# Performance work log

Measured on AMD Instinct MI355X. Metric: run time of the kernel, lower is better.

Reference implementation:

```python
import jax, jax.numpy as jnp
import numpy as np

SEQ, D_IN, D_OUT, RANK, N_ADAPTERS = 8192, 4096, 4096, 16, 8


def setup_inputs() -> dict:
    key = jax.random.key(0)
    ks = jax.random.split(key, 7)
    return {
        "x": jax.random.normal(ks[0], (SEQ, D_IN), jnp.float32),
        "weight": jax.random.normal(ks[1], (D_IN, D_OUT), jnp.float32) * (D_IN ** -0.5),
        "bias": jax.random.normal(ks[2], (D_OUT,), jnp.float32),
        "A_buffer": jax.random.normal(ks[3], (N_ADAPTERS, RANK, D_IN), jnp.float32) * (D_IN ** -0.5),
        "B_buffer": jax.random.normal(ks[4], (N_ADAPTERS, D_OUT, RANK), jnp.float32) * (RANK ** -0.5),
        "scalings": jax.random.uniform(ks[5], (SEQ,), jnp.float32, 0.5, 2.0),
        "token_indices": jax.random.randint(ks[6], (SEQ,), 0, N_ADAPTERS, jnp.int32),
    }


def reference(x, weight, bias, A_buffer, B_buffer, scalings, token_indices):
    # Base linear layer: [S, D_in] @ [D_in, D_out] + bias
    base_output = x @ weight + bias
    n_adapters = A_buffer.shape[0]
    delta = jnp.zeros_like(base_output)
    # Grouped LoRA GEMM: per-adapter small GEMMs, masked scatter back per token.
    for e in range(n_adapters):
        # run_lora_a_gemm: x @ A[e]^T with per-token scaling -> [S, rank]
        a_out = (x @ A_buffer[e].T) * scalings[:, None]
        # run_lora_b_gemm: a_out @ B[e]^T -> [S, D_out]
        b_out = a_out @ B_buffer[e].T
        delta = delta + jnp.where((token_indices == e)[:, None], b_out, 0.0)
    return base_output + delta
```

## Files before the change

### kernel.cpp

```cpp
#include <hip/hip_runtime.h>
#include <hip/hip_bf16.h>
#include <cstdint>

#define SEQ   8192
#define DIN   4096
#define DOUT  4096
#define RANK  16
#define NAD   8
#define KC    (DIN + NAD*RANK)

using f32x4  = __attribute__((ext_vector_type(4))) float;
using bf16x8 = __attribute__((ext_vector_type(8))) short;

__device__ __forceinline__ unsigned short f2bf(float f) {
  union { float f; uint32_t u; } v; v.f = f;
  return (unsigned short)((v.u + 0x7fffu + ((v.u >> 16) & 1u)) >> 16);
}

__device__ __forceinline__ void async_copy16(void* lds, const void* gmem) {
  __builtin_amdgcn_global_load_lds(
      (__attribute__((address_space(1))) void*)(uintptr_t)gmem,
      (__attribute__((address_space(3))) void*)(uint32_t)(uintptr_t)lds,
      16, 0, 0);
}


__global__ void cvt_x_kernel(const float* __restrict__ x, unsigned short* __restrict__ xcat) {
  const int64_t nchunks = (int64_t)SEQ * DIN / 8;
  for (int64_t c = (int64_t)blockIdx.x * blockDim.x + threadIdx.x; c < nchunks;
       c += (int64_t)gridDim.x * blockDim.x) {
    int64_t base = c * 8;
    int s = (int)(base >> 12);
    int k = (int)(base & (DIN - 1));
    float4 p = *(const float4*)(x + base);
    float4 q = *(const float4*)(x + base + 4);
    union { unsigned short h[8]; int4 v; } o;
    o.h[0]=f2bf(p.x); o.h[1]=f2bf(p.y); o.h[2]=f2bf(p.z); o.h[3]=f2bf(p.w);
    o.h[4]=f2bf(q.x); o.h[5]=f2bf(q.y); o.h[6]=f2bf(q.z); o.h[7]=f2bf(q.w);
    *(int4*)(xcat + (int64_t)s * KC + k) = o.v;
  }
}

__global__ void cvt_a_kernel(const float* __restrict__ a, unsigned short* __restrict__ abf) {
  int c = blockIdx.x * 256 + threadIdx.x;
  int64_t base = (int64_t)c * 8;
  float4 p = *(const float4*)(a + base);
  float4 q = *(const float4*)(a + base + 4);
  union { unsigned short h[8]; int4 v; } o;
  o.h[0]=f2bf(p.x); o.h[1]=f2bf(p.y); o.h[2]=f2bf(p.z); o.h[3]=f2bf(p.w);
  o.h[4]=f2bf(q.x); o.h[5]=f2bf(q.y); o.h[6]=f2bf(q.z); o.h[7]=f2bf(q.w);
  *(int4*)(abf + base) = o.v;
}

__global__ void cvt_w_kernel(const float* __restrict__ w, unsigned short* __restrict__ wcat) {
  int t  = threadIdx.x;
  int bn = blockIdx.x & 127;
  int bk = blockIdx.x >> 7;
  int n = bn * 32 + (t & 31);
  int k = bk * 64 + (t >> 5) * 8;
  union { unsigned short h[8]; int4 v; } o;
#pragma unroll
  for (int j = 0; j < 8; j++)
    o.h[j] = f2bf(w[(int64_t)(k + j) * DOUT + n]);
  *(int4*)(wcat + (int64_t)n * KC + k) = o.v;
}

__global__ void cvt_b_kernel(const float* __restrict__ Bbuf, unsigned short* __restrict__ wcat) {
  int idx = blockIdx.x * 256 + threadIdx.x;
  int n = idx >> 7, er = idx & 127;
  int e = er >> 4, r = er & 15;
  float v = Bbuf[((int64_t)e * DOUT + n) * RANK + r];
  wcat[(int64_t)n * KC + DIN + er] = f2bf(v);
}

__global__ __launch_bounds__(256) void gemm_lora_a(
    const unsigned short* __restrict__ A,
    const unsigned short* __restrict__ Bb,
    float* __restrict__ aout) {
  constexpr int BK = 64;
  __shared__ unsigned short sA[64 * BK];
  __shared__ unsigned short sB[128 * BK];
  int tid = threadIdx.x, wave = tid >> 6, lane = tid & 63;
  int quad = lane >> 4, l16 = lane & 15;
  int mb = blockIdx.x & 127;
  int sp = blockIdx.x >> 7;
  int row0 = mb * 64;
  int kbase = sp * (DIN / 2);
  int wm = wave >> 1, wn = wave & 1;
  int f8 = l16 & 7;

  const f32x4 zero = {0.f, 0.f, 0.f, 0.f};
  f32x4 acc[2][4];
#pragma unroll
  for (int i = 0; i < 2; i++)
#pragma unroll
    for (int j = 0; j < 4; j++) acc[i][j] = zero;

  for (int kt = 0; kt < (DIN / 2) / BK; ++kt) {
    int k0 = kbase + kt * BK;
#pragma unroll
    for (int i = 0; i < 2; i++) {
      int c = i * 256 + tid;
      int r = c >> 3, kc = ((c & 7) ^ (r & 7)) * 8;
      async_copy16(&sA[c * 8], A + (int64_t)(row0 + r) * KC + k0 + kc);
    }
#pragma unroll
    for (int i = 0; i < 4; i++) {
      int c = i * 256 + tid;
      int r = c >> 3, kc = ((c & 7) ^ (r & 7)) * 8;
      async_copy16(&sB[c * 8], Bb + (int64_t)r * DIN + k0 + kc);
    }
    __syncthreads();
#pragma unroll
    for (int ks = 0; ks < 2; ks++) {
      bf16x8 af[2], bfr[4];
      int qq = ks * 4 + quad;
      int qp = (qq ^ f8) * 8;
#pragma unroll
      for (int mi = 0; mi < 2; mi++)
        af[mi] = *(const bf16x8*)&sA[(wm * 32 + mi * 16 + l16) * BK + qp];
#pragma unroll
      for (int ni = 0; ni < 4; ni++)
        bfr[ni] = *(const bf16x8*)&sB[(wn * 64 + ni * 16 + l16) * BK + qp];
#pragma unroll
      for (int mi = 0; mi < 2; mi++)
#pragma unroll
        for (int ni = 0; ni < 4; ni++)
          acc[mi][ni] = __builtin_amdgcn_mfma_f32_16x16x32_bf16(af[mi], bfr[ni], acc[mi][ni], 0, 0, 0);
    }
    __syncthreads();
  }

  float* op = aout + (int64_t)sp * SEQ * 128;
#pragma unroll
  for (int ni = 0; ni < 4; ni++) {
    int er = wn * 64 + ni * 16 + l16;
#pragma unroll
    for (int mi = 0; mi < 2; mi++) {
      int s0 = row0 + wm * 32 + mi * 16 + quad * 4;
#pragma unroll
      for (int r = 0; r < 4; r++)
        op[(int64_t)(s0 + r) * 128 + er] = acc[mi][ni][r];
    }
  }
}

__global__ void lora_combine(const float* __restrict__ aout, const float* __restrict__ scal,
                             const int* __restrict__ tok, unsigned short* __restrict__ xcat) {
  int idx = blockIdx.x * 256 + threadIdx.x;
  int s = idx >> 7, er = idx & 127;
  float v = aout[idx] + aout[idx + (int64_t)SEQ * 128];
  v *= scal[s];
  v = ((er >> 4) == tok[s]) ? v : 0.0f;
  xcat[(int64_t)s * KC + DIN + er] = f2bf(v);
}


#define CFENCE asm volatile("" ::: "memory")

template<int MQ, int NQ>
__device__ __forceinline__ void ds_loads(const unsigned short* aT, const unsigned short* bT,
                                         int wm, int wn, int l16, int quad,
                                         bf16x8 (&af)[4][2], bf16x8 (&bfr)[2][2]) {
  int f8 = l16 & 7;
#pragma unroll
  for (int ks = 0; ks < 2; ks++) {
    int qp = ((ks * 4 + quad) ^ f8) * 8;
#pragma unroll
    for (int mi = 0; mi < 4; mi++)
      af[mi][ks] = *(const bf16x8*)&aT[(wm * 128 + MQ * 64 + mi * 16 + l16) * 64 + qp];
#pragma unroll
    for (int ni = 0; ni < 2; ni++)
      bfr[ni][ks] = *(const bf16x8*)&bT[(wn * 64 + NQ * 32 + ni * 16 + l16) * 64 + qp];
  }
}

template<int MQ, int NQ>
__device__ __forceinline__ void mfma_quad(f32x4 (&acc)[8][4], bf16x8 (&af)[4][2], bf16x8 (&bfr)[2][2]) {
  __builtin_amdgcn_s_setprio(1);
#pragma unroll
  for (int mi = 0; mi < 4; mi++)
#pragma unroll
    for (int ni = 0; ni < 2; ni++)
#pragma unroll
      for (int ks = 0; ks < 2; ks++)
        acc[MQ * 4 + mi][NQ * 2 + ni] = __builtin_amdgcn_mfma_f32_16x16x32_bf16(
            af[mi][ks], bfr[ni][ks], acc[MQ * 4 + mi][NQ * 2 + ni], 0, 0, 0);
  __builtin_amdgcn_s_setprio(0);
}

__device__ __forceinline__ void stage_A(unsigned short* sAb, const unsigned short* Ag,
                                        int mq, int k0, int tid) {
  int rr  = tid >> 3;
  int q8  = (tid & 7) * 8;
  int qc8 = ((tid & 7) ^ (rr & 7)) * 8;
  int r0 = mq * 64 + rr;
  async_copy16(sAb + r0 * 64 + q8, Ag + (int64_t)r0 * KC + k0 + qc8);
  int r1 = r0 + 128;
  async_copy16(sAb + r1 * 64 + q8, Ag + (int64_t)r1 * KC + k0 + qc8);
}

__device__ __forceinline__ void stage_B(unsigned short* sBb, const unsigned short* Bg,
                                        int nq, int k0, int tid) {
  int rB  = ((tid >> 3) & 31) | ((tid >> 8) << 6);
  int q8  = (tid & 7) * 8;
  int qc8 = ((tid & 7) ^ ((tid >> 3) & 7)) * 8;
  int r0 = nq * 32 + rB;
  async_copy16(sBb + r0 * 64 + q8, Bg + (int64_t)r0 * KC + k0 + qc8);
  int r1 = r0 + 128;
  async_copy16(sBb + r1 * 64 + q8, Bg + (int64_t)r1 * KC + k0 + qc8);
}

#define PHASE(MQ, NQ, aT, bT, STAGE_STMT)                        \
  ds_loads<MQ, NQ>(aT, bT, wm, wn, l16, quad, af, bfr);          \
  STAGE_STMT;                                                    \
  CFENCE; __builtin_amdgcn_s_barrier();                          \
  asm volatile("s_waitcnt lgkmcnt(0)" ::: "memory");             \
  mfma_quad<MQ, NQ>(acc, af, bfr)

#define ENDPHASE  CFENCE; __builtin_amdgcn_s_barrier(); CFENCE

__global__ __launch_bounds__(512, 2) void gemm_main8(
    const unsigned short* __restrict__ A,
    const unsigned short* __restrict__ B,
    const float* __restrict__ bias,
    float* __restrict__ out) {
  extern __shared__ unsigned short smem[];
  unsigned short* a0 = smem;
  unsigned short* b0 = smem + 16384;
  unsigned short* a1 = smem + 32768;
  unsigned short* b1 = smem + 49152;

  int tid = threadIdx.x, wave = tid >> 6, lane = tid & 63;
  int quad = lane >> 4, l16 = lane & 15;
  int wm = wave >> 2, wn = wave & 3;

  int bid = blockIdx.x;
  int cid = (bid & 7) * 64 + (bid >> 3);
  int bm = cid >> 4, bn = cid & 15;
  int row0 = bm * 256, col0 = bn * 256;

  const unsigned short* Ag = A + (int64_t)row0 * KC;
  const unsigned short* Bg = B + (int64_t)col0 * KC;

  const f32x4 zero = {0.f, 0.f, 0.f, 0.f};
  f32x4 acc[8][4];
#pragma unroll
  for (int i = 0; i < 8; i++)
#pragma unroll
    for (int j = 0; j < 4; j++) acc[i][j] = zero;

  bf16x8 af[4][2], bfr[2][2];

  stage_A(a0, Ag, 0, 0, tid);
  stage_B(b0, Bg, 0, 0, tid);
  stage_A(a0, Ag, 1, 0, tid);
  stage_B(b0, Bg, 1, 0, tid);
  stage_A(a1, Ag, 0, 64, tid);
  stage_B(b1, Bg, 0, 64, tid);
  asm volatile("s_waitcnt vmcnt(4)" ::: "memory");
  ENDPHASE;

  for (int tp = 0; tp < 32; ++tp) {
    int kE  = tp * 128;
    int kO  = kE + 64;
    int kE2 = kE + 128;
    int kO2 = kE + 192;
    PHASE(0, 0, a0, b0, stage_A(a1, Ag, 1, kO,  tid)); ENDPHASE;
    PHASE(0, 1, a0, b0, stage_B(b1, Bg, 1, kO,  tid)); ENDPHASE;
    PHASE(1, 0, a0, b0, stage_A(a0, Ag, 0, kE2, tid)); ENDPHASE;
    PHASE(1, 1, a0, b0, stage_B(b0, Bg, 0, kE2, tid));
    asm volatile("s_waitcnt vmcnt(4)" ::: "memory");
    ENDPHASE;
    PHASE(0, 0, a1, b1, stage_A(a0, Ag, 1, kE2, tid)); ENDPHASE;
    PHASE(0, 1, a1, b1, stage_B(b0, Bg, 1, kE2, tid)); ENDPHASE;
    PHASE(1, 0, a1, b1, stage_A(a1, Ag, 0, kO2, tid)); ENDPHASE;
    PHASE(1, 1, a1, b1, stage_B(b1, Bg, 0, kO2, tid));
    asm volatile("s_waitcnt vmcnt(4)" ::: "memory");
    ENDPHASE;
  }

  PHASE(0, 0, a0, b0, stage_A(a1, Ag, 1, 4160, tid)); ENDPHASE;
  PHASE(0, 1, a0, b0, stage_B(b1, Bg, 1, 4160, tid)); ENDPHASE;
  PHASE(1, 0, a0, b0, ((void)0)); ENDPHASE;
  PHASE(1, 1, a0, b0, ((void)0));
  asm volatile("s_waitcnt vmcnt(0)" ::: "memory");
  ENDPHASE;
  PHASE(0, 0, a1, b1, ((void)0)); ENDPHASE;
  PHASE(0, 1, a1, b1, ((void)0)); ENDPHASE;
  PHASE(1, 0, a1, b1, ((void)0)); ENDPHASE;
  PHASE(1, 1, a1, b1, ((void)0));

#pragma unroll
  for (int ni = 0; ni < 4; ni++) {
    int col = col0 + wn * 64 + ni * 16 + l16;
    float bv = bias[col];
#pragma unroll
    for (int mi = 0; mi < 8; mi++) {
      int rbase = row0 + wm * 128 + mi * 16 + quad * 4;
#pragma unroll
      for (int r = 0; r < 4; r++)
        out[(int64_t)(rbase + r) * DOUT + col] = acc[mi][ni][r] + bv;
    }
  }
}

__global__ void fb_aout(const float* __restrict__ x, const float* __restrict__ Abuf,
                        const float* __restrict__ scal, const int* __restrict__ tok,
                        float* __restrict__ aout) {
  int s = blockIdx.x;
  int e = tok[s];
  __shared__ float red[256];
  for (int r = 0; r < RANK; ++r) {
    float p = 0.f;
    for (int k = threadIdx.x; k < DIN; k += 256)
      p += x[(int64_t)s * DIN + k] * Abuf[((int64_t)e * RANK + r) * DIN + k];
    red[threadIdx.x] = p;
    __syncthreads();
    for (int off = 128; off > 0; off >>= 1) {
      if (threadIdx.x < off) red[threadIdx.x] += red[threadIdx.x + off];
      __syncthreads();
    }
    if (threadIdx.x == 0) aout[s * RANK + r] = red[0] * scal[s];
    __syncthreads();
  }
}
__global__ void fb_out(const float* __restrict__ x, const float* __restrict__ w,
                       const float* __restrict__ bias, const float* __restrict__ Bbuf,
                       const int* __restrict__ tok, const float* __restrict__ aout,
                       float* __restrict__ out) {
  int64_t idx = (int64_t)blockIdx.x * blockDim.x + threadIdx.x;
  int s = (int)(idx >> 12), n = (int)(idx & (DOUT - 1));
  float accv = bias[n];
  for (int k = 0; k < DIN; ++k)
    accv += x[(int64_t)s * DIN + k] * w[(int64_t)k * DOUT + n];
  int e = tok[s];
  float d = 0.f;
  for (int r = 0; r < RANK; ++r)
    d += aout[s * RANK + r] * Bbuf[((int64_t)e * DOUT + n) * RANK + r];
  out[idx] = accv + d;
}

extern "C" void kernel_launch(void* const* d_in, const int* in_sizes, int n_in,
                              void* d_out, int out_size, void* d_ws, size_t ws_size,
                              hipStream_t stream) {
  const float* x    = (const float*)d_in[0];
  const float* w    = (const float*)d_in[1];
  const float* bias = (const float*)d_in[2];
  const float* Abuf = (const float*)d_in[3];
  const float* Bbuf = (const float*)d_in[4];
  const float* scal = (const float*)d_in[5];
  const int*   tok  = (const int*)d_in[6];
  float* out = (float*)d_out;

  const size_t xcat_b = (size_t)SEQ * KC * 2;
  const size_t wcat_b = (size_t)DOUT * KC * 2;
  const size_t abf_b  = (size_t)NAD * RANK * DIN * 2;
  const size_t aout_b = (size_t)2 * SEQ * 128 * 4;

  if (ws_size >= xcat_b + wcat_b + abf_b + aout_b) {
    static bool lds_attr_done = false;
    if (!lds_attr_done) {
      (void)hipFuncSetAttribute((const void*)gemm_main8,
                                hipFuncAttributeMaxDynamicSharedMemorySize, 131072);
      lds_attr_done = true;
    }
    unsigned short* xcat = (unsigned short*)d_ws;
    unsigned short* wcat = (unsigned short*)((char*)d_ws + xcat_b);
    unsigned short* abf  = (unsigned short*)((char*)d_ws + xcat_b + wcat_b);
    float*          aout = (float*)((char*)d_ws + xcat_b + wcat_b + abf_b);
    cvt_x_kernel<<<4096, 256, 0, stream>>>(x, xcat);
    cvt_w_kernel<<<8192, 256, 0, stream>>>(w, wcat);
    cvt_b_kernel<<<(DOUT * 128) / 256, 256, 0, stream>>>(Bbuf, wcat);
    cvt_a_kernel<<<(NAD * RANK * DIN / 8) / 256, 256, 0, stream>>>(Abuf, abf);
    gemm_lora_a<<<256, 256, 0, stream>>>(xcat, abf, aout);
    lora_combine<<<(SEQ * 128) / 256, 256, 0, stream>>>(aout, scal, tok, xcat);
    gemm_main8<<<512, 512, 131072, stream>>>(xcat, wcat, bias, out);
  } else {
    float* aout = (float*)d_ws;
    fb_aout<<<SEQ, 256, 0, stream>>>(x, Abuf, scal, tok, aout);
    fb_out<<<(int)(((int64_t)SEQ * DOUT) / 256), 256, 0, stream>>>(x, w, bias, Bbuf, tok, aout, out);
  }
}
```

Before: 579.8 us.

## Reuse LDS fragments across quadrants with serpentine MFMA order and fewer barriers

Splits the LDS fragment loads into separate A and B loads and walks the four quadrants in a serpentine order (00, 01, 11, 10), so B and A fragments held in registers are reused and each K-tile does fewer ds_reads. The fourth quadrant needs no LDS load, so its mid-barrier is dropped. The global-to-LDS staging order and the vmcnt waits are reworked to match. The cost is an extra B fragment register set, which adds register pressure, and a more delicate async-copy/barrier schedule.

Result: faster. 546.9 us (-5.7%).

```diff
diff --git a/kernel.cpp b/kernel.cpp
--- a/kernel.cpp
+++ b/kernel.cpp
@@ -158,10 +158,9 @@
 
 #define CFENCE asm volatile("" ::: "memory")
 
-template<int MQ, int NQ>
-__device__ __forceinline__ void ds_loads(const unsigned short* aT, const unsigned short* bT,
-                                         int wm, int wn, int l16, int quad,
-                                         bf16x8 (&af)[4][2], bf16x8 (&bfr)[2][2]) {
+template<int MQ>
+__device__ __forceinline__ void ldsA(const unsigned short* aT, int wm, int l16, int quad,
+                                     bf16x8 (&af)[4][2]) {
   int f8 = l16 & 7;
 #pragma unroll
   for (int ks = 0; ks < 2; ks++) {
@@ -169,14 +168,25 @@
 #pragma unroll
     for (int mi = 0; mi < 4; mi++)
       af[mi][ks] = *(const bf16x8*)&aT[(wm * 128 + MQ * 64 + mi * 16 + l16) * 64 + qp];
+  }
+}
+
+template<int NQ>
+__device__ __forceinline__ void ldsB(const unsigned short* bT, int wn, int l16, int quad,
+                                     bf16x8 (&bq)[2][2]) {
+  int f8 = l16 & 7;
+#pragma unroll
+  for (int ks = 0; ks < 2; ks++) {
+    int qp = ((ks * 4 + quad) ^ f8) * 8;
 #pragma unroll
     for (int ni = 0; ni < 2; ni++)
-      bfr[ni][ks] = *(const bf16x8*)&bT[(wn * 64 + NQ * 32 + ni * 16 + l16) * 64 + qp];
+      bq[ni][ks] = *(const bf16x8*)&bT[(wn * 64 + NQ * 32 + ni * 16 + l16) * 64 + qp];
   }
 }
 
 template<int MQ, int NQ>
-__device__ __forceinline__ void mfma_quad(f32x4 (&acc)[8][4], bf16x8 (&af)[4][2], bf16x8 (&bfr)[2][2]) {
+__device__ __forceinline__ void mfma_quad(f32x4 (&acc)[8][4], bf16x8 (&af)[4][2],
+                                          bf16x8 (&bq)[2][2]) {
   __builtin_amdgcn_s_setprio(1);
 #pragma unroll
   for (int mi = 0; mi < 4; mi++)
@@ -185,7 +195,7 @@
 #pragma unroll
       for (int ks = 0; ks < 2; ks++)
         acc[MQ * 4 + mi][NQ * 2 + ni] = __builtin_amdgcn_mfma_f32_16x16x32_bf16(
-            af[mi][ks], bfr[ni][ks], acc[MQ * 4 + mi][NQ * 2 + ni], 0, 0, 0);
+            af[mi][ks], bq[ni][ks], acc[MQ * 4 + mi][NQ * 2 + ni], 0, 0, 0);
   __builtin_amdgcn_s_setprio(0);
 }
 
@@ -211,14 +221,29 @@
   async_copy16(sBb + r1 * 64 + q8, Bg + (int64_t)r1 * KC + k0 + qc8);
 }
 
-#define PHASE(MQ, NQ, aT, bT, STAGE_STMT)                        \
-  ds_loads<MQ, NQ>(aT, bT, wm, wn, l16, quad, af, bfr);          \
-  STAGE_STMT;                                                    \
-  CFENCE; __builtin_amdgcn_s_barrier();                          \
-  asm volatile("s_waitcnt lgkmcnt(0)" ::: "memory");             \
-  mfma_quad<MQ, NQ>(acc, af, bfr)
-
-#define ENDPHASE  CFENCE; __builtin_amdgcn_s_barrier(); CFENCE
+#define MIDBAR                                                    \
+  CFENCE; __builtin_amdgcn_s_barrier();                           \
+  asm volatile("s_waitcnt lgkmcnt(0)" ::: "memory")
+#define ENDBAR  CFENCE; __builtin_amdgcn_s_barrier(); CFENCE
+
+#define TILE(aT, bT, S0, S1, S2, S3, BND)                         \
+  ldsA<0>(aT, wm, l16, quad, af);                                 \
+  ldsB<0>(bT, wn, l16, quad, bf0);                                \
+  S0; MIDBAR;                                                     \
+  mfma_quad<0, 0>(acc, af, bf0);                                  \
+  ENDBAR;                                                         \
+  ldsB<1>(bT, wn, l16, quad, bf1);                                \
+  S1; MIDBAR;                                                     \
+  mfma_quad<0, 1>(acc, af, bf1);                                  \
+  ENDBAR;                                                         \
+  ldsA<1>(aT, wm, l16, quad, af);                                 \
+  S2; MIDBAR;                                                     \
+  mfma_quad<1, 1>(acc, af, bf1);                                  \
+  ENDBAR;                                                         \
+  S3; CFENCE;                                                     \
+  mfma_quad<1, 0>(acc, af, bf0);                                  \
+  BND;                                                            \
+  ENDBAR
 
 __global__ __launch_bounds__(512, 2) void gemm_main8(
     const unsigned short* __restrict__ A,
@@ -250,46 +275,49 @@
 #pragma unroll
     for (int j = 0; j < 4; j++) acc[i][j] = zero;
 
-  bf16x8 af[4][2], bfr[2][2];
+  bf16x8 af[4][2], bf0[2][2], bf1[2][2];
 
   stage_A(a0, Ag, 0, 0, tid);
   stage_B(b0, Bg, 0, 0, tid);
+  stage_B(b0, Bg, 1, 0, tid);
   stage_A(a0, Ag, 1, 0, tid);
-  stage_B(b0, Bg, 1, 0, tid);
   stage_A(a1, Ag, 0, 64, tid);
-  stage_B(b1, Bg, 0, 64, tid);
-  asm volatile("s_waitcnt vmcnt(4)" ::: "memory");
-  ENDPHASE;
+  stage_B(b1, Bg, 1, 64, tid);
+  stage_A(a1, Ag, 1, 64, tid);
+  asm volatile("s_waitcnt vmcnt(6)" ::: "memory");
+  ENDBAR;
+
+#define BND6 asm volatile("s_waitcnt vmcnt(6)" ::: "memory")
 
   for (int tp = 0; tp < 32; ++tp) {
-    int kE  = tp * 128;
-    int kO  = kE + 64;
-    int kE2 = kE + 128;
-    int kO2 = kE + 192;
-    PHASE(0, 0, a0, b0, stage_A(a1, Ag, 1, kO,  tid)); ENDPHASE;
-    PHASE(0, 1, a0, b0, stage_B(b1, Bg, 1, kO,  tid)); ENDPHASE;
-    PHASE(1, 0, a0, b0, stage_A(a0, Ag, 0, kE2, tid)); ENDPHASE;
-    PHASE(1, 1, a0, b0, stage_B(b0, Bg, 0, kE2, tid));
-    asm volatile("s_waitcnt vmcnt(4)" ::: "memory");
-    ENDPHASE;
-    PHASE(0, 0, a1, b1, stage_A(a0, Ag, 1, kE2, tid)); ENDPHASE;
-    PHASE(0, 1, a1, b1, stage_B(b0, Bg, 1, kE2, tid)); ENDPHASE;
-    PHASE(1, 0, a1, b1, stage_A(a1, Ag, 0, kO2, tid)); ENDPHASE;
-    PHASE(1, 1, a1, b1, stage_B(b1, Bg, 0, kO2, tid));
-    asm volatile("s_waitcnt vmcnt(4)" ::: "memory");
-    ENDPHASE;
-  }
-
-  PHASE(0, 0, a0, b0, stage_A(a1, Ag, 1, 4160, tid)); ENDPHASE;
-  PHASE(0, 1, a0, b0, stage_B(b1, Bg, 1, 4160, tid)); ENDPHASE;
-  PHASE(1, 0, a0, b0, ((void)0)); ENDPHASE;
-  PHASE(1, 1, a0, b0, ((void)0));
-  asm volatile("s_waitcnt vmcnt(0)" ::: "memory");
-  ENDPHASE;
-  PHASE(0, 0, a1, b1, ((void)0)); ENDPHASE;
-  PHASE(0, 1, a1, b1, ((void)0)); ENDPHASE;
-  PHASE(1, 0, a1, b1, ((void)0)); ENDPHASE;
-  PHASE(1, 1, a1, b1, ((void)0));
+    int kE = tp * 128;
+    TILE(a0, b0,
+         stage_B(b1, Bg, 0, kE + 64,  tid),
+         stage_A(a0, Ag, 0, kE + 128, tid),
+         stage_B(b0, Bg, 1, kE + 128, tid),
+         stage_A(a0, Ag, 1, kE + 128, tid),
+         BND6);
+    TILE(a1, b1,
+         stage_B(b0, Bg, 0, kE + 128, tid),
+         stage_A(a1, Ag, 0, kE + 192, tid),
+         stage_B(b1, Bg, 1, kE + 192, tid),
+         stage_A(a1, Ag, 1, kE + 192, tid),
+         BND6);
+  }
+
+  TILE(a0, b0,
+       stage_B(b1, Bg, 0, 4160, tid),
+       (void)0, (void)0, (void)0,
+       asm volatile("s_waitcnt vmcnt(0)" ::: "memory"));
+
+  ldsA<0>(a1, wm, l16, quad, af);
+  ldsB<0>(b1, wn, l16, quad, bf0);
+  mfma_quad<0, 0>(acc, af, bf0);
+  ldsB<1>(b1, wn, l16, quad, bf1);
+  mfma_quad<0, 1>(acc, af, bf1);
+  ldsA<1>(a1, wm, l16, quad, af);
+  mfma_quad<1, 1>(acc, af, bf1);
+  mfma_quad<1, 0>(acc, af, bf0);
 
 #pragma unroll
   for (int ni = 0; ni < 4; ni++) {
```
